# Kernel optimization log

Hardware: AMD Instinct MI355X
Metric: run time of the kernel (lower is better)

Reference implementation:

```python
import jax, jax.numpy as jnp
import numpy as np

B, T, D = 2, 2048, 1024
NH, DH = 16, 64  # inner = NH*DH = D
SCALE_INIT = 0.02


def setup_inputs() -> dict:
    key = jax.random.key(0)
    kx, kq, kk, kv, ko = jax.random.split(key, 5)
    return {
        "x": jax.random.normal(kx, (B, T, D), dtype=jnp.float32),
        "Wq": jax.random.normal(kq, (D, NH * DH), dtype=jnp.float32) * SCALE_INIT,
        "Wk": jax.random.normal(kk, (D, NH * DH), dtype=jnp.float32) * SCALE_INIT,
        "Wv": jax.random.normal(kv, (D, NH * DH), dtype=jnp.float32) * SCALE_INIT,
        "Wo": jax.random.normal(ko, (NH * DH, D), dtype=jnp.float32) * SCALE_INIT,
    }


def reference(x, Wq, Wk, Wv, Wo):
    # x: (B, T, D)
    b, t, _ = x.shape

    def split_heads(h):
        # (B, T, NH*DH) -> (B, NH, T, DH)
        return h.reshape(b, t, NH, DH).transpose(0, 2, 1, 3)

    q = split_heads(x @ Wq)
    k = split_heads(x @ Wk)
    v = split_heads(x @ Wv)

    scale = jnp.asarray(1.0 / np.sqrt(DH), dtype=x.dtype)
    # The per-chunk loop in the original is mathematically equivalent to
    # full causal attention: each query row attends to keys with k_pos <= q_pos.
    scores = jnp.einsum("bhqd,bhkd->bhqk", q, k) * scale  # (B, NH, T, T)
    causal_mask = jnp.arange(t)[None, :] > jnp.arange(t)[:, None]  # k_pos > q_pos
    scores = jnp.where(causal_mask, -jnp.inf, scores)
    attn = jax.nn.softmax(scores, axis=-1)
    attn = jnp.nan_to_num(attn)  # matches torch.nan_to_num (no fully-masked rows in causal case)
    o = jnp.einsum("bhqk,bhkd->bhqd", attn, v)  # (B, NH, T, DH)
    o = o.transpose(0, 2, 1, 3).reshape(b, t, NH * DH)  # merge heads
    return o @ Wo  # (B, T, D)
```

## Files before the change

### kernel.cpp

```cpp
#include <hip/hip_runtime.h>

#define Bsz 2
#define Tsz 2048
#define Dsz 1024
#define NHsz 16
#define Msz (Bsz*Tsz)

typedef unsigned short bfu;
typedef __attribute__((ext_vector_type(8))) short short8;
typedef __attribute__((ext_vector_type(4))) short short4v;
typedef __attribute__((ext_vector_type(4))) float floatx4;

__device__ __forceinline__ bfu f2bf(float f) {
  unsigned int u = __builtin_bit_cast(unsigned int, f);
  u += 0x7fffu + ((u >> 16) & 1u);
  return (bfu)(u >> 16);
}

__device__ __forceinline__ void async16(const void* g, void* l) {
  void* gnc = (void*)g;
  __builtin_amdgcn_global_load_lds((__attribute__((address_space(1))) void*)gnc,
                                   (__attribute__((address_space(3))) void*)l,
                                   16, 0, 0);
}

__global__ __launch_bounds__(256) void convert_x(const float* __restrict__ x,
                                                 bfu* __restrict__ xb) {
  int i = blockIdx.x * 256 + threadIdx.x;
  float4 v = ((const float4*)x)[i];
  short4v o;
  o[0] = (short)f2bf(v.x); o[1] = (short)f2bf(v.y);
  o[2] = (short)f2bf(v.z); o[3] = (short)f2bf(v.w);
  *(short4v*)(xb + (size_t)i * 4) = o;
}

__global__ __launch_bounds__(256) void transpose_w(const float* __restrict__ W0, const float* __restrict__ W1,
                                                   const float* __restrict__ W2, const float* __restrict__ W3,
                                                   bfu* __restrict__ wt) {
  __shared__ float tile[32][33];
  const float* W = blockIdx.z == 0 ? W0 : blockIdx.z == 1 ? W1 : blockIdx.z == 2 ? W2 : W3;
  bfu* WT = wt + (size_t)blockIdx.z * Dsz * Dsz;
  int tx = threadIdx.x, ty = threadIdx.y;
  int kb = blockIdx.y * 32, nb = blockIdx.x * 32;
#pragma unroll
  for (int i = 0; i < 4; ++i)
    tile[ty + i*8][tx] = W[(size_t)(kb + ty + i*8) * Dsz + nb + tx];
  __syncthreads();
#pragma unroll
  for (int i = 0; i < 4; ++i)
    WT[(size_t)(nb + ty + i*8) * Dsz + kb + tx] = f2bf(tile[tx][ty + i*8]);
}

template <bool F32OUT>
__global__ __launch_bounds__(256) void gemm128(const bfu* __restrict__ A, const bfu* __restrict__ Bt0,
                                               void* __restrict__ C0, int K, int N,
                                               size_t strideB, size_t strideC, float scale0) {
  const int tid = threadIdx.x, wave = tid >> 6, lane = tid & 63;
  const int g = lane >> 4, c = lane & 15;
  const int m0 = blockIdx.y * 128, n0 = blockIdx.x * 128;
  const bfu* Bt = Bt0 + strideB * blockIdx.z;
  const float scale = (blockIdx.z == 0) ? scale0 : 1.0f;
  __shared__ bfu As[128 * 32];
  __shared__ bfu Bs[128 * 32];
  floatx4 acc[4][4] = {};
  const int srow = lane >> 2, scol = (lane & 3) * 8;
  const bfu* gA = A  + (size_t)(m0 + srow) * K + scol;
  const bfu* gB = Bt + (size_t)(n0 + srow) * K + scol;
  const int wm = (wave >> 1) * 64, wn = (wave & 1) * 64;
  for (int k0 = 0; k0 < K; k0 += 32) {
    __syncthreads();
#pragma unroll
    for (int cc = 0; cc < 2; ++cc) {
      const int chunk = wave * 2 + cc;
      async16(gA + (size_t)chunk * 16 * K + k0, &As[chunk * 512]);
      async16(gB + (size_t)chunk * 16 * K + k0, &Bs[chunk * 512]);
    }
    __syncthreads();
    short8 afr[4], bfr[4];
#pragma unroll
    for (int t = 0; t < 4; ++t) afr[t] = *(const short8*)&As[(wm + t*16 + c) * 32 + g * 8];
#pragma unroll
    for (int t = 0; t < 4; ++t) bfr[t] = *(const short8*)&Bs[(wn + t*16 + c) * 32 + g * 8];
#pragma unroll
    for (int i = 0; i < 4; ++i)
#pragma unroll
      for (int j = 0; j < 4; ++j)
        acc[i][j] = __builtin_amdgcn_mfma_f32_16x16x32_bf16(afr[i], bfr[j], acc[i][j], 0, 0, 0);
  }
  const bool vtrans = (!F32OUT) && (blockIdx.z == 2);
#pragma unroll
  for (int i = 0; i < 4; ++i) {
#pragma unroll
    for (int j = 0; j < 4; ++j) {
      const int m = m0 + wm + i*16 + g*4;
      const int n = n0 + wn + j*16 + c;
      if (vtrans) {
        bfu* vtp = (bfu*)C0 + (size_t)2 * strideC;
        size_t o = ((size_t)((m >> 11) * 16 + (n >> 6)) * 64 + (n & 63)) * Tsz + (m & 2047);
        short4v pk;
#pragma unroll
        for (int r = 0; r < 4; ++r) pk[r] = (short)f2bf(acc[i][j][r]);
        *(short4v*)&vtp[o] = pk;
      } else {
#pragma unroll
        for (int r = 0; r < 4; ++r) {
          float v = acc[i][j][r] * scale;
          if (F32OUT) ((float*)C0)[(size_t)(m + r) * N + n] = v;
          else        ((bfu*)C0)[strideC * blockIdx.z + (size_t)(m + r) * N + n] = f2bf(v);
        }
      }
    }
  }
}

__global__ __launch_bounds__(256, 2) void attn_kernel(const bfu* __restrict__ qkv,
                                                      bfu* __restrict__ obuf) {
  const int tid = threadIdx.x, wave = tid >> 6, lane = tid & 63;
  const int g = (lane >> 4) & 3, c = lane & 15, c7 = c & 7;
  const int bh = blockIdx.y, b = bh >> 4, h = bh & 15;
  const size_t hb = (size_t)b * Tsz * Dsz + h * 64;
  const bfu* Qp = qkv + hb;
  const bfu* Kp = qkv + (size_t)Msz * Dsz + hb;
  const bfu* Vt = qkv + (size_t)2 * Msz * Dsz + (size_t)bh * 64 * Tsz;

  __shared__ bfu Ks[128 * 64];
  __shared__ bfu Vs[64 * 128];
  __shared__ bfu Ps[4][16 * 128];

  const int kst_row = lane >> 3;
  const int kst_off = ((lane & 7) ^ kst_row) << 3;
  const int vst_row = lane >> 4;

  for (int half = 0; half < 2; ++half) {
    const int j = half ? (31 - (int)blockIdx.x) : (int)blockIdx.x;
    const int qw = j * 64 + wave * 16;
    const int ktm = j >> 1;

    short8 bq[2];
#pragma unroll
    for (int kk = 0; kk < 2; ++kk)
      bq[kk] = *(const short8*)(Qp + (size_t)(qw + c) * Dsz + kk * 32 + g * 8);

    floatx4 acc[4] = {};
    float mi = -3.0e38f, li = 0.0f;

    for (int kt = 0; kt <= ktm; ++kt) {
      __syncthreads();
#pragma unroll
      for (int cc = 0; cc < 4; ++cc) {
        const int ch = wave * 4 + cc;
        async16(Kp + (size_t)(kt * 128 + ch * 8 + kst_row) * Dsz + kst_off, &Ks[ch * 512]);
        const int drow = ch * 4 + vst_row;
        async16(Vt + (size_t)drow * Tsz + kt * 128 + (((lane & 15) ^ (drow & 7)) << 3), &Vs[ch * 512]);
      }
      __syncthreads();

      floatx4 st[8] = {};
#pragma unroll
      for (int kk = 0; kk < 2; ++kk)
#pragma unroll
        for (int mk = 0; mk < 8; ++mk) {
          const short8 kf = *(const short8*)&Ks[(mk * 16 + c) * 64 + (((kk * 4 + g) ^ c7) << 3)];
          st[mk] = __builtin_amdgcn_mfma_f32_16x16x32_bf16(kf, bq[kk], st[mk], 0, 0, 0);
        }

      if (kt == ktm) {
#pragma unroll
        for (int mk = 0; mk < 8; ++mk) {
          const int keyb = kt * 128 + mk * 16 + g * 4;
#pragma unroll
          for (int r = 0; r < 4; ++r)
            if (keyb + r > qw + c) st[mk][r] = -1.0e38f;
        }
      }

      float mloc = -3.0e38f;
#pragma unroll
      for (int mk = 0; mk < 8; ++mk)
#pragma unroll
        for (int r = 0; r < 4; ++r) mloc = fmaxf(mloc, st[mk][r]);
      mloc = fmaxf(mloc, __shfl_xor(mloc, 16));
      mloc = fmaxf(mloc, __shfl_xor(mloc, 32));
      const float mnew = fmaxf(mi, mloc);
      const float alpha = exp2f(mi - mnew);
      mi = mnew;
      float sum = 0.0f;
#pragma unroll
      for (int mk = 0; mk < 8; ++mk) {
        short4v pk;
#pragma unroll
        for (int r = 0; r < 4; ++r) {
          const float p = exp2f(st[mk][r] - mnew);
          sum += p;
          pk[r] = (short)f2bf(p);
        }
        *(short4v*)&Ps[wave][c * 128 + (((mk * 2 + (g >> 1)) ^ c7) << 3) + ((g & 1) << 2)] = pk;
      }
      sum += __shfl_xor(sum, 16);
      sum += __shfl_xor(sum, 32);
      li = li * alpha + sum;

      float al[4];
#pragma unroll
      for (int r = 0; r < 4; ++r) al[r] = __shfl(alpha, (lane & 48) | (g * 4 + r));
#pragma unroll
      for (int nd = 0; nd < 4; ++nd)
#pragma unroll
        for (int r = 0; r < 4; ++r) acc[nd][r] *= al[r];

#pragma unroll
      for (int kc = 0; kc < 4; ++kc) {
        const int sl = ((kc * 4 + g) ^ c7) << 3;
        const short8 pf = *(const short8*)&Ps[wave][c * 128 + sl];
#pragma unroll
        for (int nd = 0; nd < 4; ++nd) {
          const short8 vf = *(const short8*)&Vs[(nd * 16 + c) * 128 + sl];
          acc[nd] = __builtin_amdgcn_mfma_f32_16x16x32_bf16(pf, vf, acc[nd], 0, 0, 0);
        }
      }
    }

    float inv[4];
#pragma unroll
    for (int r = 0; r < 4; ++r) inv[r] = 1.0f / __shfl(li, (lane & 48) | (g * 4 + r));
#pragma unroll
    for (int nd = 0; nd < 4; ++nd)
#pragma unroll
      for (int r = 0; r < 4; ++r)
        obuf[(size_t)(b * Tsz + qw + g * 4 + r) * Dsz + h * 64 + nd * 16 + c] =
            f2bf(acc[nd][r] * inv[r]);
  }
}

extern "C" void kernel_launch(void* const* d_in, const int* in_sizes, int n_in,
                              void* d_out, int out_size, void* d_ws, size_t ws_size,
                              hipStream_t stream) {
  const float* x  = (const float*)d_in[0];
  const float* Wq = (const float*)d_in[1];
  const float* Wk = (const float*)d_in[2];
  const float* Wv = (const float*)d_in[3];
  const float* Wo = (const float*)d_in[4];
  float* out = (float*)d_out;

  bfu* xb   = (bfu*)d_ws;
  bfu* wt   = xb  + (size_t)Msz * Dsz;
  bfu* qkv  = wt  + (size_t)4 * Dsz * Dsz;
  bfu* obuf = qkv + (size_t)3 * Msz * Dsz;

  convert_x<<<dim3(Msz * Dsz / (256 * 4)), dim3(256), 0, stream>>>(x, xb);
  transpose_w<<<dim3(32, 32, 4), dim3(32, 8), 0, stream>>>(Wq, Wk, Wv, Wo, wt);
  gemm128<false><<<dim3(Dsz / 128, Msz / 128, 3), dim3(256), 0, stream>>>(
      xb, wt, (void*)qkv, Dsz, Dsz, (size_t)Dsz * Dsz, (size_t)Msz * Dsz,
      0.125f * 1.44269504088896f);
  attn_kernel<<<dim3(16, Bsz * NHsz), dim3(256), 0, stream>>>(qkv, obuf);
  gemm128<true><<<dim3(Dsz / 128, Msz / 128, 1), dim3(256), 0, stream>>>(
      obuf, wt + (size_t)3 * Dsz * Dsz, (void*)out, Dsz, Dsz, (size_t)0, (size_t)0, 1.0f);
}
```

Measured before the change: 206.4 us.

## Restructure attention: 128-query blocks, double-buffered K/V, diagonal-tile MFMA skipping

The attention kernel now gives each block a single 128-query tile, with each wave handling 32 queries. This replaces the old pairing of two 64-query halves. The grid is a flat 512 blocks, ordered so the heaviest tiles launch first. K/V tiles are double-buffered in LDS so the next tile's async loads overlap compute, and K fragments are loaded once and reused across both query fragments. On the diagonal tile, fully masked MFMA sub-tiles are skipped, and bf16 packing uses a paired hardware conversion. The costs are double the LDS use and higher register pressure, which may lower occupancy.

```diff
diff --git a/kernel.cpp b/kernel.cpp
--- a/kernel.cpp
+++ b/kernel.cpp
@@ -1,4 +1,6 @@
 #include <hip/hip_runtime.h>
+#include <hip/hip_bf16.h>
+#include <string.h>
 
 #define Bsz 2
 #define Tsz 2048
@@ -15,6 +17,15 @@
   unsigned int u = __builtin_bit_cast(unsigned int, f);
   u += 0x7fffu + ((u >> 16) & 1u);
   return (bfu)(u >> 16);
+}
+
+__device__ __forceinline__ short4v pack4bf(float a, float b, float c_, float d) {
+  __hip_bfloat162 h01 = __float22bfloat162_rn(make_float2(a, b));
+  __hip_bfloat162 h23 = __float22bfloat162_rn(make_float2(c_, d));
+  uint2 uu;
+  memcpy(&uu.x, &h01, 4);
+  memcpy(&uu.y, &h23, 4);
+  return __builtin_bit_cast(short4v, uu);
 }
 
 __device__ __forceinline__ void async16(const void* g, void* l) {
@@ -117,118 +128,155 @@
                                                       bfu* __restrict__ obuf) {
   const int tid = threadIdx.x, wave = tid >> 6, lane = tid & 63;
   const int g = (lane >> 4) & 3, c = lane & 15, c7 = c & 7;
-  const int bh = blockIdx.y, b = bh >> 4, h = bh & 15;
+  const int lin = blockIdx.x;
+  const int bh = lin & 31, p = (lin >> 5) & 7;
+  const int j = (lin < 256) ? (15 - p) : p;
+  const int b = bh >> 4, h = bh & 15;
   const size_t hb = (size_t)b * Tsz * Dsz + h * 64;
   const bfu* Qp = qkv + hb;
   const bfu* Kp = qkv + (size_t)Msz * Dsz + hb;
   const bfu* Vt = qkv + (size_t)2 * Msz * Dsz + (size_t)bh * 64 * Tsz;
 
-  __shared__ bfu Ks[128 * 64];
-  __shared__ bfu Vs[64 * 128];
+  __shared__ bfu Ks[2][128 * 64];
+  __shared__ bfu Vs[2][64 * 128];
   __shared__ bfu Ps[4][16 * 128];
 
   const int kst_row = lane >> 3;
   const int kst_off = ((lane & 7) ^ kst_row) << 3;
   const int vst_row = lane >> 4;
 
-  for (int half = 0; half < 2; ++half) {
-    const int j = half ? (31 - (int)blockIdx.x) : (int)blockIdx.x;
-    const int qw = j * 64 + wave * 16;
-    const int ktm = j >> 1;
-
-    short8 bq[2];
+  const int qw = j * 128 + wave * 32;
+
+  short8 bq[2][2];
+#pragma unroll
+  for (int qf = 0; qf < 2; ++qf)
 #pragma unroll
     for (int kk = 0; kk < 2; ++kk)
-      bq[kk] = *(const short8*)(Qp + (size_t)(qw + c) * Dsz + kk * 32 + g * 8);
-
-    floatx4 acc[4] = {};
-    float mi = -3.0e38f, li = 0.0f;
-
-    for (int kt = 0; kt <= ktm; ++kt) {
-      __syncthreads();
+      bq[qf][kk] = *(const short8*)(Qp + (size_t)(qw + qf*16 + c) * Dsz + kk*32 + g*8);
+
+  floatx4 acc[2][4] = {};
+  float mi[2] = {-3.0e38f, -3.0e38f}, li[2] = {0.0f, 0.0f};
+
+#pragma unroll
+  for (int cc = 0; cc < 4; ++cc) {
+    const int ch = wave * 4 + cc;
+    async16(Kp + (size_t)(ch*8 + kst_row) * Dsz + kst_off, &Ks[0][ch * 512]);
+    const int drow = ch * 4 + vst_row;
+    async16(Vt + (size_t)drow * Tsz + (((lane & 15) ^ (drow & 7)) << 3), &Vs[0][ch * 512]);
+  }
+  __syncthreads();
+
+  for (int kt = 0; kt <= j; ++kt) {
+    const int cur = kt & 1;
+    if (kt < j) {
 #pragma unroll
       for (int cc = 0; cc < 4; ++cc) {
         const int ch = wave * 4 + cc;
-        async16(Kp + (size_t)(kt * 128 + ch * 8 + kst_row) * Dsz + kst_off, &Ks[ch * 512]);
+        async16(Kp + (size_t)((kt+1)*128 + ch*8 + kst_row) * Dsz + kst_off, &Ks[cur ^ 1][ch * 512]);
         const int drow = ch * 4 + vst_row;
-        async16(Vt + (size_t)drow * Tsz + kt * 128 + (((lane & 15) ^ (drow & 7)) << 3), &Vs[ch * 512]);
-      }
-      __syncthreads();
-
-      floatx4 st[8] = {};
-#pragma unroll
-      for (int kk = 0; kk < 2; ++kk)
-#pragma unroll
-        for (int mk = 0; mk < 8; ++mk) {
-          const short8 kf = *(const short8*)&Ks[(mk * 16 + c) * 64 + (((kk * 4 + g) ^ c7) << 3)];
-          st[mk] = __builtin_amdgcn_mfma_f32_16x16x32_bf16(kf, bq[kk], st[mk], 0, 0, 0);
-        }
-
-      if (kt == ktm) {
-#pragma unroll
-        for (int mk = 0; mk < 8; ++mk) {
-          const int keyb = kt * 128 + mk * 16 + g * 4;
-#pragma unroll
-          for (int r = 0; r < 4; ++r)
-            if (keyb + r > qw + c) st[mk][r] = -1.0e38f;
-        }
+        async16(Vt + (size_t)drow * Tsz + (kt+1)*128 + (((lane & 15) ^ (drow & 7)) << 3),
+                &Vs[cur ^ 1][ch * 512]);
+      }
+    }
+
+    short8 kfr[2][8];
+#pragma unroll
+    for (int kk = 0; kk < 2; ++kk)
+#pragma unroll
+      for (int mk = 0; mk < 8; ++mk)
+        kfr[kk][mk] = *(const short8*)&Ks[cur][(mk*16 + c) * 64 + (((kk*4 + g) ^ c7) << 3)];
+
+    const bool diag = (kt == j);
+#pragma unroll
+    for (int qf = 0; qf < 2; ++qf) {
+      const int wp = wave * 2 + qf;
+      const int mk_hi = diag ? (wp + 1) : 8;
+      const int kc_hi = diag ? ((wp >> 1) + 1) : 4;
+
+      floatx4 st[8];
+#pragma unroll
+      for (int mk = 0; mk < 8; ++mk) {
+        if (mk < mk_hi) {
+          floatx4 z = {};
+          z = __builtin_amdgcn_mfma_f32_16x16x32_bf16(kfr[0][mk], bq[qf][0], z, 0, 0, 0);
+          st[mk] = __builtin_amdgcn_mfma_f32_16x16x32_bf16(kfr[1][mk], bq[qf][1], z, 0, 0, 0);
+        }
+      }
+      if (diag) {
+#pragma unroll
+        for (int mk = 0; mk < 8; ++mk)
+          if (mk == wp) {
+#pragma unroll
+            for (int r = 0; r < 4; ++r)
+              if (g*4 + r > c) st[mk][r] = -1.0e38f;
+          }
       }
 
       float mloc = -3.0e38f;
 #pragma unroll
       for (int mk = 0; mk < 8; ++mk)
-#pragma unroll
-        for (int r = 0; r < 4; ++r) mloc = fmaxf(mloc, st[mk][r]);
+        if (mk < mk_hi) {
+#pragma unroll
+          for (int r = 0; r < 4; ++r) mloc = fmaxf(mloc, st[mk][r]);
+        }
       mloc = fmaxf(mloc, __shfl_xor(mloc, 16));
       mloc = fmaxf(mloc, __shfl_xor(mloc, 32));
-      const float mnew = fmaxf(mi, mloc);
-      const float alpha = exp2f(mi - mnew);
-      mi = mnew;
+      const float mnew = fmaxf(mi[qf], mloc);
+      const float alpha = exp2f(mi[qf] - mnew);
+      mi[qf] = mnew;
+
       float sum = 0.0f;
 #pragma unroll
-      for (int mk = 0; mk < 8; ++mk) {
-        short4v pk;
-#pragma unroll
-        for (int r = 0; r < 4; ++r) {
-          const float p = exp2f(st[mk][r] - mnew);
-          sum += p;
-          pk[r] = (short)f2bf(p);
-        }
-        *(short4v*)&Ps[wave][c * 128 + (((mk * 2 + (g >> 1)) ^ c7) << 3) + ((g & 1) << 2)] = pk;
+      for (int mk = 0; mk < 8; ++mk)
+        if (mk < mk_hi) {
+          float pr[4];
+#pragma unroll
+          for (int r = 0; r < 4; ++r) { pr[r] = exp2f(st[mk][r] - mnew); sum += pr[r]; }
+          *(short4v*)&Ps[wave][c * 128 + (((mk*2 + (g >> 1)) ^ c7) << 3) + ((g & 1) << 2)] =
+              pack4bf(pr[0], pr[1], pr[2], pr[3]);
+        }
+      if (diag && !(wp & 1)) {
+        short4v z4 = {};
+        *(short4v*)&Ps[wave][c * 128 + ((((wp+1)*2 + (g >> 1)) ^ c7) << 3) + ((g & 1) << 2)] = z4;
       }
       sum += __shfl_xor(sum, 16);
       sum += __shfl_xor(sum, 32);
-      li = li * alpha + sum;
+      li[qf] = li[qf] * alpha + sum;
 
       float al[4];
 #pragma unroll
-      for (int r = 0; r < 4; ++r) al[r] = __shfl(alpha, (lane & 48) | (g * 4 + r));
+      for (int r = 0; r < 4; ++r) al[r] = __shfl(alpha, (lane & 48) | (g*4 + r));
 #pragma unroll
       for (int nd = 0; nd < 4; ++nd)
 #pragma unroll
-        for (int r = 0; r < 4; ++r) acc[nd][r] *= al[r];
-
-#pragma unroll
-      for (int kc = 0; kc < 4; ++kc) {
-        const int sl = ((kc * 4 + g) ^ c7) << 3;
-        const short8 pf = *(const short8*)&Ps[wave][c * 128 + sl];
-#pragma unroll
-        for (int nd = 0; nd < 4; ++nd) {
-          const short8 vf = *(const short8*)&Vs[(nd * 16 + c) * 128 + sl];
-          acc[nd] = __builtin_amdgcn_mfma_f32_16x16x32_bf16(pf, vf, acc[nd], 0, 0, 0);
-        }
-      }
+        for (int r = 0; r < 4; ++r) acc[qf][nd][r] *= al[r];
+
+#pragma unroll
+      for (int kc = 0; kc < 4; ++kc)
+        if (kc < kc_hi) {
+          const int sl = ((kc*4 + g) ^ c7) << 3;
+          const short8 pf = *(const short8*)&Ps[wave][c * 128 + sl];
+#pragma unroll
+          for (int nd = 0; nd < 4; ++nd) {
+            const short8 vf = *(const short8*)&Vs[cur][(nd*16 + c) * 128 + sl];
+            acc[qf][nd] = __builtin_amdgcn_mfma_f32_16x16x32_bf16(pf, vf, acc[qf][nd], 0, 0, 0);
+          }
+        }
     }
-
+    __syncthreads();
+  }
+
+#pragma unroll
+  for (int qf = 0; qf < 2; ++qf) {
     float inv[4];
 #pragma unroll
-    for (int r = 0; r < 4; ++r) inv[r] = 1.0f / __shfl(li, (lane & 48) | (g * 4 + r));
+    for (int r = 0; r < 4; ++r) inv[r] = 1.0f / __shfl(li[qf], (lane & 48) | (g*4 + r));
 #pragma unroll
     for (int nd = 0; nd < 4; ++nd)
 #pragma unroll
       for (int r = 0; r < 4; ++r)
-        obuf[(size_t)(b * Tsz + qw + g * 4 + r) * Dsz + h * 64 + nd * 16 + c] =
-            f2bf(acc[nd][r] * inv[r]);
+        obuf[(size_t)(b * Tsz + qw + qf*16 + g*4 + r) * Dsz + h * 64 + nd*16 + c] =
+            f2bf(acc[qf][nd][r] * inv[r]);
   }
 }
 
@@ -252,7 +300,7 @@
   gemm128<false><<<dim3(Dsz / 128, Msz / 128, 3), dim3(256), 0, stream>>>(
       xb, wt, (void*)qkv, Dsz, Dsz, (size_t)Dsz * Dsz, (size_t)Msz * Dsz,
       0.125f * 1.44269504088896f);
-  attn_kernel<<<dim3(16, Bsz * NHsz), dim3(256), 0, stream>>>(qkv, obuf);
+  attn_kernel<<<dim3(512), dim3(256), 0, stream>>>(qkv, obuf);
   gemm128<true><<<dim3(Dsz / 128, Msz / 128, 1), dim3(256), 0, stream>>>(
       obuf, wt + (size_t)3 * Dsz * Dsz, (void*)out, Dsz, Dsz, (size_t)0, (size_t)0, 1.0f);
 }
```

New measurement: 222.6 us. +7.8%, slower.
